# Kernel optimization log

Hardware: AMD Instinct MI355X
Metric: run time of the kernel (lower is better)

The kernel has to match this reference:

```python
import jax, jax.numpy as jnp
import numpy as np

INPUT_SIZE = 784
HIDDEN_SIZE = 256
NUM_CLASSES = 10
BATCH = 32768


def setup_inputs() -> dict:
    key = jax.random.key(0)
    k_x, k_w1, k_b1, k_w2, k_b2 = jax.random.split(key, 5)
    return {
        "x": jax.random.normal(k_x, (BATCH, INPUT_SIZE), dtype=jnp.float32),
        "fc1_weight": jax.random.normal(k_w1, (HIDDEN_SIZE, INPUT_SIZE), dtype=jnp.float32),
        "fc1_bias": jax.random.normal(k_b1, (HIDDEN_SIZE,), dtype=jnp.float32),
        "fc2_weight": jax.random.normal(k_w2, (NUM_CLASSES, HIDDEN_SIZE), dtype=jnp.float32),
        "fc2_bias": jax.random.normal(k_b2, (NUM_CLASSES,), dtype=jnp.float32),
    }


def reference(x, fc1_weight, fc1_bias, fc2_weight, fc2_bias):
    # hidden = x @ W1^T + b1, ReLU
    hidden = jnp.einsum("bi,hi->bh", x, fc1_weight) + fc1_bias
    activated = jnp.maximum(hidden, 0.0)
    # output = activated @ W2^T + b2
    logits = jnp.einsum("bh,ch->bc", activated, fc2_weight) + fc2_bias
    return jax.nn.softmax(logits, axis=-1)
```

## Files before the change

### kernel.cpp

```cpp
#include <hip/hip_runtime.h>
#include <math.h>

#define BATCH_N   32768
#define IN_F      784
#define HID_F     256
#define NCLS      10
#define BM        64
#define NTHREADS  512

typedef __attribute__((ext_vector_type(8))) short short8;
typedef __attribute__((ext_vector_type(4))) float f32x4;

#define WS_W1H 0
#define WS_W1L 409600

union S8U { short8 s; uint4 u; };

__device__ __forceinline__ void cvt8(float4 a, float4 b, short8* hi, short8* lo) {
    const unsigned M = 0xFFFF0000u;
    const unsigned ux = __float_as_uint(a.x), uy = __float_as_uint(a.y),
                   uz = __float_as_uint(a.z), uw = __float_as_uint(a.w),
                   vx = __float_as_uint(b.x), vy = __float_as_uint(b.y),
                   vz = __float_as_uint(b.z), vw = __float_as_uint(b.w);
    S8U h, l;
    h.u.x = (ux >> 16) | (uy & M);
    h.u.y = (uz >> 16) | (uw & M);
    h.u.z = (vx >> 16) | (vy & M);
    h.u.w = (vz >> 16) | (vw & M);
    const float rx = a.x - __uint_as_float(ux & M);
    const float ry = a.y - __uint_as_float(uy & M);
    const float rz = a.z - __uint_as_float(uz & M);
    const float rw = a.w - __uint_as_float(uw & M);
    const float sx = b.x - __uint_as_float(vx & M);
    const float sy = b.y - __uint_as_float(vy & M);
    const float sz = b.z - __uint_as_float(vz & M);
    const float sw_ = b.w - __uint_as_float(vw & M);
    l.u.x = (__float_as_uint(rx) >> 16) | (__float_as_uint(ry) & M);
    l.u.y = (__float_as_uint(rz) >> 16) | (__float_as_uint(rw) & M);
    l.u.z = (__float_as_uint(sx) >> 16) | (__float_as_uint(sy) & M);
    l.u.w = (__float_as_uint(sz) >> 16) | (__float_as_uint(sw_) & M);
    *hi = h.s; *lo = l.s;
}

__global__ __launch_bounds__(256)
void prep_w1_kernel(const float* __restrict__ w1, char* __restrict__ ws) {
    const int s    = blockIdx.x * 256 + threadIdx.x;
    const int lane = s & 63, ct = (s >> 6) & 15, kt = s >> 10;
    const int n    = ct * 16 + (lane & 15);
    const int k0   = kt * 32 + (lane >> 4) * 8;
    float4 a = make_float4(0.f, 0.f, 0.f, 0.f), b = a;
    if (k0 + 7 < IN_F) {
        const float* p = w1 + (size_t)n * IN_F + k0;
        a = *(const float4*)p;
        b = *(const float4*)(p + 4);
    }
    short8 hi, lo;
    cvt8(a, b, &hi, &lo);
    *(short8*)(ws + WS_W1H + (size_t)s * 16) = hi;
    *(short8*)(ws + WS_W1L + (size_t)s * 16) = lo;
}

__global__ __launch_bounds__(NTHREADS, 4)
void mlp_mfma_kernel(const float* __restrict__ x,
                     const char*  __restrict__ wsb,
                     const float* __restrict__ b1,
                     const float* __restrict__ w2,
                     const float* __restrict__ b2,
                     float* __restrict__ out)
{
    __shared__ union {
        struct { short8 xh[2][1024]; short8 xl[2][1024]; } st;
        float hid[64 * 128];
    } sm;

    const int tid  = threadIdx.x;
    const int lane = tid & 63;
    const int wv   = tid >> 6;
    const int wc   = wv & 3;
    const int wr   = wv >> 2;
    const int m    = lane & 15;
    const int quad = lane >> 4;
    const int row0 = blockIdx.x * BM;

    const int slr  = tid >> 3;
    const int ks16 = tid & 7;
    const float* xs = x + (size_t)(row0 + slr) * IN_F + ks16 * 16;
    const int wb0 = slr * 16 + (((ks16 * 2)    ) ^ (slr & 7));
    const int wb1 = slr * 16 + (((ks16 * 2) + 1) ^ (slr & 7));

    const int msw = m & 7;
    const int rb0 = (wr * 32 + m) * 16;
    const int rb1 = rb0 + 256;

    const char* bhp = wsb + WS_W1H + ((size_t)(wc * 4) * 64 + lane) * 16;
    const char* blp = wsb + WS_W1L + ((size_t)(wc * 4) * 64 + lane) * 16;

    f32x4 acc[2][4];
    #pragma unroll
    for (int a = 0; a < 2; ++a)
        #pragma unroll
        for (int b = 0; b < 4; ++b)
            acc[a][b] = (f32x4){0.f, 0.f, 0.f, 0.f};

    short8 bhc[4], blc[4];
    #pragma unroll
    for (int c = 0; c < 4; ++c) {
        bhc[c] = *(const short8*)(bhp + c * 1024);
        blc[c] = *(const short8*)(blp + c * 1024);
    }
    {
        const float4 a0 = *(const float4*)(xs);
        const float4 a1 = *(const float4*)(xs + 4);
        const float4 a2 = *(const float4*)(xs + 8);
        const float4 a3 = *(const float4*)(xs + 12);
        short8 h0, l0, h1, l1;
        cvt8(a0, a1, &h0, &l0);
        cvt8(a2, a3, &h1, &l1);
        sm.st.xh[0][wb0] = h0; sm.st.xl[0][wb0] = l0;
        sm.st.xh[0][wb1] = h1; sm.st.xl[0][wb1] = l1;
    }
    __syncthreads();

    int cur = 0;
    for (int r = 0; r < 6; ++r) {
        const short8* xhr = sm.st.xh[cur];
        const short8* xlr = sm.st.xl[cur];
        const int k0n = (r + 1) * 128 + ks16 * 16;
        float4 xa0 = make_float4(0.f, 0.f, 0.f, 0.f), xa1 = xa0, xa2 = xa0, xa3 = xa0;
        if (k0n < IN_F) {
            const float* p = xs + (r + 1) * 128;
            xa0 = *(const float4*)(p);
            xa1 = *(const float4*)(p + 4);
            xa2 = *(const float4*)(p + 8);
            xa3 = *(const float4*)(p + 12);
        }
        #pragma unroll
        for (int ktl = 0; ktl < 4; ++ktl) {
            const int kt = r * 4 + ktl;
            short8 bhn[4], bln[4];
            #pragma unroll
            for (int c = 0; c < 4; ++c) {
                bhn[c] = *(const short8*)(bhp + (size_t)(kt + 1) * 16384 + c * 1024);
                bln[c] = *(const short8*)(blp + (size_t)(kt + 1) * 16384 + c * 1024);
            }
            __builtin_amdgcn_s_setprio(1);
            #pragma unroll
            for (int rt = 0; rt < 2; ++rt) {
                const int sl = (rt ? rb1 : rb0) + ((ktl * 4 + quad) ^ msw);
                const short8 ah = xhr[sl];
                const short8 al = xlr[sl];
                #pragma unroll
                for (int c = 0; c < 4; ++c) {
                    acc[rt][c] = __builtin_amdgcn_mfma_f32_16x16x32_bf16(ah, bhc[c], acc[rt][c], 0, 0, 0);
                    acc[rt][c] = __builtin_amdgcn_mfma_f32_16x16x32_bf16(al, bhc[c], acc[rt][c], 0, 0, 0);
                    acc[rt][c] = __builtin_amdgcn_mfma_f32_16x16x32_bf16(ah, blc[c], acc[rt][c], 0, 0, 0);
                }
            }
            __builtin_amdgcn_s_setprio(0);
            #pragma unroll
            for (int c = 0; c < 4; ++c) { bhc[c] = bhn[c]; blc[c] = bln[c]; }
        }
        {
            short8 h0, l0, h1, l1;
            cvt8(xa0, xa1, &h0, &l0);
            cvt8(xa2, xa3, &h1, &l1);
            short8* xhw = sm.st.xh[cur ^ 1];
            short8* xlw = sm.st.xl[cur ^ 1];
            xhw[wb0] = h0; xlw[wb0] = l0;
            xhw[wb1] = h1; xlw[wb1] = l1;
        }
        __syncthreads();
        cur ^= 1;
    }

    {
        const short8* xhr = sm.st.xh[cur];
        const short8* xlr = sm.st.xl[cur];
        __builtin_amdgcn_s_setprio(1);
        #pragma unroll
        for (int rt = 0; rt < 2; ++rt) {
            const int sl = (rt ? rb1 : rb0) + (quad ^ msw);
            const short8 ah = xhr[sl];
            const short8 al = xlr[sl];
            #pragma unroll
            for (int c = 0; c < 4; ++c) {
                acc[rt][c] = __builtin_amdgcn_mfma_f32_16x16x32_bf16(ah, bhc[c], acc[rt][c], 0, 0, 0);
                acc[rt][c] = __builtin_amdgcn_mfma_f32_16x16x32_bf16(al, bhc[c], acc[rt][c], 0, 0, 0);
                acc[rt][c] = __builtin_amdgcn_mfma_f32_16x16x32_bf16(ah, blc[c], acc[rt][c], 0, 0, 0);
            }
        }
        __builtin_amdgcn_s_setprio(0);
    }

    const int rl    = tid >> 3;
    const int slice = tid & 7;
    const int gb    = (slice >> 1) * 64 + (slice & 1) * 16;
    const int cb    = slice * 16;
    const int sw2   = (rl & 7) << 2;

    float lg[NCLS];
    #pragma unroll
    for (int k = 0; k < NCLS; ++k) lg[k] = 0.f;

    #pragma unroll
    for (int p = 0; p < 2; ++p) {
        __syncthreads();
        #pragma unroll
        for (int cl = 0; cl < 2; ++cl) {
            const int c  = 2 * p + cl;
            const int g  = (wc * 4 + c) * 16 + m;
            const float bv = b1[g];
            const int cc = wc * 32 + cl * 16 + m;
            #pragma unroll
            for (int rt = 0; rt < 2; ++rt)
                #pragma unroll
                for (int reg = 0; reg < 4; ++reg) {
                    const int row = wr * 32 + rt * 16 + quad * 4 + reg;
                    sm.hid[row * 128 + (cc ^ ((row & 7) << 2))] =
                        fmaxf(acc[rt][c][reg] + bv, 0.f);
                }
        }
        __syncthreads();
        #pragma unroll
        for (int i = 0; i < 4; ++i) {
            const float4 h = *(const float4*)(sm.hid + rl * 128 + ((cb + i * 4) ^ sw2));
            const int g4 = gb + 32 * p + i * 4;
            #pragma unroll
            for (int k = 0; k < NCLS; ++k) {
                const float4 w = *(const float4*)(w2 + k * HID_F + g4);
                lg[k] += h.x * w.x + h.y * w.y + h.z * w.z + h.w * w.w;
            }
        }
    }

    #pragma unroll
    for (int k = 0; k < NCLS; ++k) {
        float v = lg[k];
        v += __shfl_xor(v, 1);
        v += __shfl_xor(v, 2);
        v += __shfl_xor(v, 4);
        lg[k] = v + b2[k];
    }
    float mx = -1e30f;
    #pragma unroll
    for (int k = 0; k < NCLS; ++k) mx = fmaxf(mx, lg[k]);
    float s = 0.f;
    #pragma unroll
    for (int k = 0; k < NCLS; ++k) { lg[k] = __expf(lg[k] - mx); s += lg[k]; }
    const float inv = 1.f / s;
    const float va = (slice & 4)
        ? ((slice & 2) ? ((slice & 1) ? lg[7] : lg[6]) : ((slice & 1) ? lg[5] : lg[4]))
        : ((slice & 2) ? ((slice & 1) ? lg[3] : lg[2]) : ((slice & 1) ? lg[1] : lg[0]));
    const float vb = (slice & 1) ? lg[9] : lg[8];
    float* o = out + (size_t)(row0 + rl) * NCLS;
    o[slice] = va * inv;
    if (slice < 2) o[8 + slice] = vb * inv;
}

extern "C" void kernel_launch(void* const* d_in, const int* in_sizes, int n_in,
                              void* d_out, int out_size, void* d_ws, size_t ws_size,
                              hipStream_t stream)
{
    const float* x  = (const float*)d_in[0];
    const float* w1 = (const float*)d_in[1];
    const float* b1 = (const float*)d_in[2];
    const float* w2 = (const float*)d_in[3];
    const float* b2 = (const float*)d_in[4];
    float* out = (float*)d_out;

    hipLaunchKernelGGL(prep_w1_kernel, dim3(100), dim3(256), 0, stream,
                       w1, (char*)d_ws);
    hipLaunchKernelGGL(mlp_mfma_kernel, dim3(BATCH_N / BM), dim3(NTHREADS), 0, stream,
                       x, (const char*)d_ws, b1, w2, b2, out);
}
```

Measured before the change: 225.2 us.

## Stream x tiles directly into LDS via global_load_lds with 4-stage ring

Replaces the register-staged x load and bf16 split-and-store with direct global-to-LDS async loads of raw fp32 x into a 4-slot ring buffer. The hi/lo bf16 conversion now happens after the LDS read, and synchronisation uses explicit vmcnt waits and s_barrier every k-tile instead of every 128 columns. This aims to hide global latency and remove register pressure and VALU work from the load path. In exchange, occupancy bounds drop from 4 to 2 blocks, LDS traffic grows because fp32 is stored, and the conversion is repeated by each wave that reads the tile.

```diff
diff --git a/kernel.cpp b/kernel.cpp
--- a/kernel.cpp
+++ b/kernel.cpp
@@ -60,7 +60,19 @@
     *(short8*)(ws + WS_W1L + (size_t)s * 16) = lo;
 }
 
-__global__ __launch_bounds__(NTHREADS, 4)
+__device__ __forceinline__ void gload16(const void* g, void* l) {
+    __builtin_amdgcn_global_load_lds(
+        (const __attribute__((address_space(1))) void*)g,
+        (__attribute__((address_space(3))) void*)l, 16, 0, 0);
+}
+
+__device__ __forceinline__ short8 gload_s8(const void* p) {
+    short8 r;
+    asm volatile("global_load_dwordx4 %0, %1, off" : "=v"(r) : "v"(p));
+    return r;
+}
+
+__global__ __launch_bounds__(NTHREADS, 2)
 void mlp_mfma_kernel(const float* __restrict__ x,
                      const char*  __restrict__ wsb,
                      const float* __restrict__ b1,
@@ -68,10 +80,8 @@
                      const float* __restrict__ b2,
                      float* __restrict__ out)
 {
-    __shared__ union {
-        struct { short8 xh[2][1024]; short8 xl[2][1024]; } st;
-        float hid[64 * 128];
-    } sm;
+    __shared__ char  xraw[4][8192];
+    __shared__ float hid[64 * 128];
 
     const int tid  = threadIdx.x;
     const int lane = tid & 63;
@@ -82,15 +92,14 @@
     const int quad = lane >> 4;
     const int row0 = blockIdx.x * BM;
 
-    const int slr  = tid >> 3;
-    const int ks16 = tid & 7;
-    const float* xs = x + (size_t)(row0 + slr) * IN_F + ks16 * 16;
-    const int wb0 = slr * 16 + (((ks16 * 2)    ) ^ (slr & 7));
-    const int wb1 = slr * 16 + (((ks16 * 2) + 1) ^ (slr & 7));
+    const int srow = wv * 8 + (lane >> 3);
+    const int gch  = (lane & 7) ^ (lane >> 3);
+    const float* xg = x + (size_t)(row0 + srow) * IN_F;
 
     const int msw = m & 7;
-    const int rb0 = (wr * 32 + m) * 16;
-    const int rb1 = rb0 + 256;
+    const int rowbase = (wr * 32 + m) * 128;
+    const int o0 = ((2 * quad)     ^ msw) * 16;
+    const int o1 = ((2 * quad + 1) ^ msw) * 16;
 
     const char* bhp = wsb + WS_W1H + ((size_t)(wc * 4) * 64 + lane) * 16;
     const char* blp = wsb + WS_W1L + ((size_t)(wc * 4) * 64 + lane) * 16;
@@ -102,53 +111,41 @@
         for (int b = 0; b < 4; ++b)
             acc[a][b] = (f32x4){0.f, 0.f, 0.f, 0.f};
 
-    short8 bhc[4], blc[4];
+    gload16(xg + gch * 4,      &xraw[0][wv * 1024]);
+    gload16(xg + 32 + gch * 4, &xraw[1][wv * 1024]);
+    short8 bhc[4], blc[4], bhn[4], bln[4];
     #pragma unroll
     for (int c = 0; c < 4; ++c) {
-        bhc[c] = *(const short8*)(bhp + c * 1024);
-        blc[c] = *(const short8*)(blp + c * 1024);
-    }
-    {
-        const float4 a0 = *(const float4*)(xs);
-        const float4 a1 = *(const float4*)(xs + 4);
-        const float4 a2 = *(const float4*)(xs + 8);
-        const float4 a3 = *(const float4*)(xs + 12);
-        short8 h0, l0, h1, l1;
-        cvt8(a0, a1, &h0, &l0);
-        cvt8(a2, a3, &h1, &l1);
-        sm.st.xh[0][wb0] = h0; sm.st.xl[0][wb0] = l0;
-        sm.st.xh[0][wb1] = h1; sm.st.xl[0][wb1] = l1;
-    }
-    __syncthreads();
-
-    int cur = 0;
-    for (int r = 0; r < 6; ++r) {
-        const short8* xhr = sm.st.xh[cur];
-        const short8* xlr = sm.st.xl[cur];
-        const int k0n = (r + 1) * 128 + ks16 * 16;
-        float4 xa0 = make_float4(0.f, 0.f, 0.f, 0.f), xa1 = xa0, xa2 = xa0, xa3 = xa0;
-        if (k0n < IN_F) {
-            const float* p = xs + (r + 1) * 128;
-            xa0 = *(const float4*)(p);
-            xa1 = *(const float4*)(p + 4);
-            xa2 = *(const float4*)(p + 8);
-            xa3 = *(const float4*)(p + 12);
-        }
-        #pragma unroll
-        for (int ktl = 0; ktl < 4; ++ktl) {
-            const int kt = r * 4 + ktl;
-            short8 bhn[4], bln[4];
+        bhc[c] = gload_s8(bhp + c * 1024);
+        blc[c] = gload_s8(blp + c * 1024);
+    }
+
+    for (int kb = 0; kb < 24; kb += 4) {
+        #pragma unroll
+        for (int i = 0; i < 4; ++i) {
+            const int kt = kb + i;
+            {
+                const int ktc = (kt + 2 > 24) ? 24 : kt + 2;
+                const int cgc = (ktc == 24 && gch > 3) ? 0 : gch;
+                gload16(xg + ktc * 32 + cgc * 4, &xraw[(i + 2) & 3][wv * 1024]);
+            }
             #pragma unroll
             for (int c = 0; c < 4; ++c) {
-                bhn[c] = *(const short8*)(bhp + (size_t)(kt + 1) * 16384 + c * 1024);
-                bln[c] = *(const short8*)(blp + (size_t)(kt + 1) * 16384 + c * 1024);
-            }
+                bhn[c] = gload_s8(bhp + (size_t)(kt + 1) * 16384 + c * 1024);
+                bln[c] = gload_s8(blp + (size_t)(kt + 1) * 16384 + c * 1024);
+            }
+            asm volatile("s_waitcnt vmcnt(9)");
+            __builtin_amdgcn_sched_barrier(0);
+            __builtin_amdgcn_s_barrier();
+            __builtin_amdgcn_sched_barrier(0);
+            const char* xr = &xraw[i][0];
             __builtin_amdgcn_s_setprio(1);
             #pragma unroll
             for (int rt = 0; rt < 2; ++rt) {
-                const int sl = (rt ? rb1 : rb0) + ((ktl * 4 + quad) ^ msw);
-                const short8 ah = xhr[sl];
-                const short8 al = xlr[sl];
+                const float4 fa = *(const float4*)(xr + rowbase + rt * 2048 + o0);
+                const float4 fb = *(const float4*)(xr + rowbase + rt * 2048 + o1);
+                short8 ah, al;
+                cvt8(fa, fb, &ah, &al);
                 #pragma unroll
                 for (int c = 0; c < 4; ++c) {
                     acc[rt][c] = __builtin_amdgcn_mfma_f32_16x16x32_bf16(ah, bhc[c], acc[rt][c], 0, 0, 0);
@@ -160,28 +157,25 @@
             #pragma unroll
             for (int c = 0; c < 4; ++c) { bhc[c] = bhn[c]; blc[c] = bln[c]; }
         }
-        {
-            short8 h0, l0, h1, l1;
-            cvt8(xa0, xa1, &h0, &l0);
-            cvt8(xa2, xa3, &h1, &l1);
-            short8* xhw = sm.st.xh[cur ^ 1];
-            short8* xlw = sm.st.xl[cur ^ 1];
-            xhw[wb0] = h0; xlw[wb0] = l0;
-            xhw[wb1] = h1; xlw[wb1] = l1;
-        }
-        __syncthreads();
-        cur ^= 1;
     }
 
     {
-        const short8* xhr = sm.st.xh[cur];
-        const short8* xlr = sm.st.xl[cur];
+        asm volatile("s_waitcnt vmcnt(0)");
+        __builtin_amdgcn_sched_barrier(0);
+        __builtin_amdgcn_s_barrier();
+        __builtin_amdgcn_sched_barrier(0);
+        const char* xr = &xraw[0][0];
         __builtin_amdgcn_s_setprio(1);
         #pragma unroll
         for (int rt = 0; rt < 2; ++rt) {
-            const int sl = (rt ? rb1 : rb0) + (quad ^ msw);
-            const short8 ah = xhr[sl];
-            const short8 al = xlr[sl];
+            const float4 fa = *(const float4*)(xr + rowbase + rt * 2048 + o0);
+            const float4 fb = *(const float4*)(xr + rowbase + rt * 2048 + o1);
+            short8 ah, al;
+            cvt8(fa, fb, &ah, &al);
+            if (quad >= 2) {
+                const short8 zz = {0, 0, 0, 0, 0, 0, 0, 0};
+                ah = zz; al = zz;
+            }
             #pragma unroll
             for (int c = 0; c < 4; ++c) {
                 acc[rt][c] = __builtin_amdgcn_mfma_f32_16x16x32_bf16(ah, bhc[c], acc[rt][c], 0, 0, 0);
@@ -204,7 +198,7 @@
 
     #pragma unroll
     for (int p = 0; p < 2; ++p) {
-        __syncthreads();
+        if (p) __syncthreads();
         #pragma unroll
         for (int cl = 0; cl < 2; ++cl) {
             const int c  = 2 * p + cl;
@@ -216,14 +210,14 @@
                 #pragma unroll
                 for (int reg = 0; reg < 4; ++reg) {
                     const int row = wr * 32 + rt * 16 + quad * 4 + reg;
-                    sm.hid[row * 128 + (cc ^ ((row & 7) << 2))] =
+                    hid[row * 128 + (cc ^ ((row & 7) << 2))] =
                         fmaxf(acc[rt][c][reg] + bv, 0.f);
                 }
         }
         __syncthreads();
         #pragma unroll
         for (int i = 0; i < 4; ++i) {
-            const float4 h = *(const float4*)(sm.hid + rl * 128 + ((cb + i * 4) ^ sw2));
+            const float4 h = *(const float4*)(hid + rl * 128 + ((cb + i * 4) ^ sw2));
             const int g4 = gb + 32 * p + i * 4;
             #pragma unroll
             for (int k = 0; k < NCLS; ++k) {
```

After: 215.8 us. 1.04x faster.
